# Performance work log

Measured on AMD Instinct MI355X. Metric: run time of the kernel, lower is better.

The kernel has to match this reference:

```python
import jax, jax.numpy as jnp
import numpy as np
from functools import partial

VOCAB, EMB, HID, B, T, K = 30000, 256, 512, 128, 256, 12
START, STOP = 10, 11


def lstm_scan(xs, mask, W_ih, W_hh, b_ih, b_hh, h0, c0):
    """xs: [T,B,E], mask: [T,B] bool. PyTorch gate order i,f,g,o. Masked steps carry state (packed-seq semantics)."""
    def step(carry, inp):
        h, c = carry
        x_t, m_t = inp
        gates = x_t @ W_ih.T + h @ W_hh.T + (b_ih + b_hh)  # [B,4H]
        i, f, g, o = jnp.split(gates, 4, axis=-1)
        c_new = jax.nn.sigmoid(f) * c + jax.nn.sigmoid(i) * jnp.tanh(g)
        h_new = jax.nn.sigmoid(o) * jnp.tanh(c_new)
        m = m_t[:, None]
        h = jnp.where(m, h_new, h)
        c = jnp.where(m, c_new, c)
        return (h, c), h
    _, hs = jax.lax.scan(step, (h0, c0), (xs, mask))
    return hs  # [T,B,H]


def crf_log_partition(emissions, mask, trans):
    """emissions: [T,B,K], mask: [T,B]. Vectorized log-sum-exp forward algorithm."""
    b, k = emissions.shape[1], emissions.shape[2]
    alpha0 = jnp.full((b, k), -10000.0, emissions.dtype).at[:, START].set(0.0)
    def step(alpha, inp):
        emit_t, m_t = inp
        # alpha_new[b,j] = logsumexp_i(alpha[b,i] + trans[j,i]) + emit[b,j]
        scores = alpha[:, None, :] + trans[None, :, :]  # [B,Knext,Kprev]
        alpha_new = jax.nn.logsumexp(scores, axis=-1) + emit_t
        return jnp.where(m_t[:, None], alpha_new, alpha), None
    alpha, _ = jax.lax.scan(step, alpha0, (emissions, mask))
    return jax.nn.logsumexp(alpha + trans[STOP][None, :], axis=-1)  # [B]


def crf_gold_score(emissions_bt, tags, lengths, trans):
    """emissions_bt: [B,T,K]. Gold path score with <start> prepended and <stop> transition."""
    b, t = tags.shape
    tags_ext = jnp.concatenate([jnp.full((b, 1), START, tags.dtype), tags], axis=1)  # [B,T+1]
    prev, nxt = tags_ext[:, :-1], tags_ext[:, 1:]  # [B,T]
    trans_s = trans[nxt, prev]  # [B,T]
    emit_s = jnp.take_along_axis(emissions_bt, nxt[:, :, None], axis=2)[:, :, 0]  # [B,T]
    valid = jnp.arange(t)[None, :] < lengths[:, None]  # [B,T]
    score = jnp.sum(jnp.where(valid, trans_s + emit_s, 0.0), axis=1)
    last_tag = jnp.take_along_axis(tags, (lengths - 1)[:, None], axis=1)[:, 0]
    return score + trans[STOP, last_tag]


def setup_inputs() -> dict:
    key = jax.random.key(0)
    ks = jax.random.split(key, 16)
    s = 0.1
    x = jax.random.randint(ks[0], (B, T), 0, VOCAB)
    lengths = jax.random.randint(ks[1], (B,), 1, T + 1)
    tags = jax.random.randint(ks[2], (B, T), 0, K - 2)  # real labels only
    embedding = jax.random.normal(ks[3], (VOCAB, EMB), jnp.float32) * s
    W_ih_f = jax.random.normal(ks[4], (4 * HID, EMB), jnp.float32) * s
    W_hh_f = jax.random.normal(ks[5], (4 * HID, HID), jnp.float32) * s
    b_ih_f = jax.random.normal(ks[6], (4 * HID,), jnp.float32) * s
    b_hh_f = jax.random.normal(ks[7], (4 * HID,), jnp.float32) * s
    W_ih_b = jax.random.normal(ks[8], (4 * HID, EMB), jnp.float32) * s
    W_hh_b = jax.random.normal(ks[9], (4 * HID, HID), jnp.float32) * s
    b_ih_b = jax.random.normal(ks[10], (4 * HID,), jnp.float32) * s
    b_hh_b = jax.random.normal(ks[11], (4 * HID,), jnp.float32) * s
    fc_W = jax.random.normal(ks[12], (K, 2 * HID), jnp.float32) * s
    fc_b = jnp.zeros((K,), jnp.float32)
    trans = jax.random.normal(ks[13], (K, K), jnp.float32) * s
    trans = trans.at[START, :].set(-10000.0).at[:, STOP].set(-10000.0)
    h0 = jax.random.normal(ks[14], (2, B, HID), jnp.float32) * s
    c0 = jax.random.normal(ks[15], (2, B, HID), jnp.float32) * s
    return dict(x=x, lengths=lengths, tags=tags, embedding=embedding,
                W_ih_f=W_ih_f, W_hh_f=W_hh_f, b_ih_f=b_ih_f, b_hh_f=b_hh_f,
                W_ih_b=W_ih_b, W_hh_b=W_hh_b, b_ih_b=b_ih_b, b_hh_b=b_hh_b,
                fc_W=fc_W, fc_b=fc_b, trans=trans, h0=h0, c0=c0)


def reference(x, lengths, tags, embedding, W_ih_f, W_hh_f, b_ih_f, b_hh_f,
              W_ih_b, W_hh_b, b_ih_b, b_hh_b, fc_W, fc_b, trans, h0, c0):
    # neg_log_likelihood: BiLSTM emission feats -> CRF logZ - gold score. Dropout = eval (identity).
    emb = embedding[x]                 # [B,T,E]
    xs = emb.transpose(1, 0, 2)        # [T,B,E] time-major
    t = xs.shape[0]
    mask = jnp.arange(t)[:, None] < lengths[None, :]  # [T,B]
    hs_f = lstm_scan(xs, mask, W_ih_f, W_hh_f, b_ih_f, b_hh_f, h0[0], c0[0])
    hs_b = lstm_scan(xs[::-1], mask[::-1], W_ih_b, W_hh_b, b_ih_b, b_hh_b, h0[1], c0[1])[::-1]
    out = jnp.concatenate([hs_f, hs_b], axis=-1)      # [T,B,2H]
    emissions = out @ fc_W.T + fc_b                    # [T,B,K]
    log_z = crf_log_partition(emissions, mask, trans)  # [B]
    gold = crf_gold_score(emissions.transpose(1, 0, 2), tags, lengths, trans)  # [B]
    return log_z - gold  # per-sentence NLL, [B]
```

## Files before the change

kernel.cpp:

```cpp
#include <hip/hip_runtime.h>
#include <hip/hip_bf16.h>

#define TT 256
#define BB 128
#define EMBD 256
#define HID 512
#define KTAG 12
#define START_TAG 10
#define STOP_TAG 11
#define SMEM_BYTES 148608

typedef __attribute__((ext_vector_type(8))) short short8;
typedef __attribute__((ext_vector_type(4))) float f32x4;

__device__ __forceinline__ unsigned short f2bf(float f) {
    union { float f; unsigned int u; } v; v.f = f;
    unsigned int r = v.u + 0x7fffu + ((v.u >> 16) & 1u);
    return (unsigned short)(r >> 16);
}
__device__ __forceinline__ float fsig(float x) {
    return __fdividef(1.0f, 1.0f + __expf(-x));
}
__device__ __forceinline__ float ftanh(float x) {
    return 2.0f * __fdividef(1.0f, 1.0f + __expf(-2.0f * x)) - 1.0f;
}
__device__ __forceinline__ void gll16(const void* g, void* l) {
    __builtin_amdgcn_global_load_lds((const __attribute__((address_space(1))) void*)g,
                                     (__attribute__((address_space(3))) void*)l, 16, 0, 0);
}
__device__ __forceinline__ void pack8(const float* src, unsigned short* dst) {
    float4 v0 = *(const float4*)src;
    float4 v1 = *(const float4*)(src + 4);
    unsigned short tmp[8];
    tmp[0] = f2bf(v0.x); tmp[1] = f2bf(v0.y); tmp[2] = f2bf(v0.z); tmp[3] = f2bf(v0.w);
    tmp[4] = f2bf(v1.x); tmp[5] = f2bf(v1.y); tmp[6] = f2bf(v1.z); tmp[7] = f2bf(v1.w);
    *(uint4*)dst = *(const uint4*)tmp;
}

#define SCHED_FENCE() __builtin_amdgcn_sched_barrier(0)
#define WAIT_VM4() do { asm volatile("s_waitcnt vmcnt(4)" ::: "memory"); SCHED_FENCE(); } while (0)
#define WAIT_VM0() do { asm volatile("s_waitcnt vmcnt(0)" ::: "memory"); SCHED_FENCE(); } while (0)
#define BARRIER_RAW() do { __builtin_amdgcn_s_barrier(); SCHED_FENCE(); } while (0)

__global__ void prologue(const int* __restrict__ x, const float* __restrict__ emb,
                         const float* __restrict__ Wihf, const float* __restrict__ Whhf,
                         const float* __restrict__ Wihb, const float* __restrict__ Whhb,
                         const float* __restrict__ h0,
                         const float* __restrict__ bihf, const float* __restrict__ bhhf,
                         const float* __restrict__ bihb, const float* __restrict__ bhhb,
                         const float* __restrict__ fcW,
                         unsigned short* __restrict__ xs, unsigned short* __restrict__ Wr,
                         unsigned short* __restrict__ h0buf, float* __restrict__ bias2,
                         unsigned short* __restrict__ fcWr, unsigned int* __restrict__ ctrl)
{
    int blk = blockIdx.x;
    int tid = threadIdx.x;
    if (blk < 4096) {
        int i = blk * 256 + tid;
        int chk = i & 31;
        int row = i >> 5;
        int b = row & (BB - 1);
        int t = row >> 7;
        pack8(emb + (size_t)x[b * TT + t] * EMBD + chk * 8, xs + (size_t)row * EMBD + chk * 8);
    } else if (blk < 5632) {
        int i = (blk - 4096) * 256 + tid;
        int c8 = i % 96;
        int r2 = i / 96;
        int nr = r2 & 2047;
        int dir = r2 >> 11;
        int utile = nr >> 6;
        int r6 = nr & 63;
        int wm = r6 >> 4;
        int rr = r6 & 15;
        int ul = rr >> 2, g = rr & 3;
        int orow = g * HID + utile * 16 + wm * 4 + ul;
        int k0 = c8 * 8;
        const float* Wih = dir ? Wihb : Wihf;
        const float* Whh = dir ? Whhb : Whhf;
        const float* src = (k0 < EMBD) ? (Wih + (size_t)orow * EMBD + k0)
                                       : (Whh + (size_t)orow * HID + (k0 - EMBD));
        pack8(src, Wr + ((size_t)dir * 2048 + nr) * 768 + k0);
    } else {
        int i = (blk - 5632) * 256 + tid;
        if (i < 2 * BB * HID) h0buf[i] = f2bf(h0[i]);
        if (i < 2 * 2048) {
            int dir = i >> 11, j = i & 2047;
            bias2[i] = dir ? (bihb[j] + bhhb[j]) : (bihf[j] + bhhf[j]);
        }
        if (i < 16 * 1024) {
            int tag = i >> 10, k = i & 1023;
            fcWr[i] = f2bf(tag < KTAG ? fcW[tag * 1024 + k] : 0.0f);
        }
        if (i < 2048) ctrl[i] = 0u;
    }
}

__launch_bounds__(256, 1)
__global__ void lstm_persistent(
    const unsigned short* __restrict__ xs, const unsigned short* __restrict__ Wr,
    const float* __restrict__ bias2, const int* __restrict__ lengths,
    const unsigned short* __restrict__ h0buf, const float* __restrict__ c0,
    unsigned short* __restrict__ hsf, unsigned short* __restrict__ hsb,
    unsigned int* __restrict__ ctrl)
{
    extern __shared__ char smem[];
    unsigned short* Wlds = (unsigned short*)smem;
    unsigned short* Abuf = (unsigned short*)(smem + 98304);
    unsigned short* hrep = (unsigned short*)(smem + 147456);

    const int blk = blockIdx.x;
    const int grp = blk & 7;
    const int dir = grp >> 2;
    const int btile = grp & 3;
    const int utile = blk >> 3;
    const int bg0 = btile * 32;

    const int tid = threadIdx.x;
    const int w = tid >> 6;
    const int l = tid & 63;
    const int l15 = l & 15, l16 = l >> 4;

    unsigned int* wflags = ctrl + 64 + grp * 128;
    unsigned int* myflag = wflags + utile * 4 + w;

    unsigned short* hs = dir ? hsb : hsf;
    unsigned int* hs_u32 = (unsigned int*)hs;

    {
        const unsigned short* src0 =
            Wr + ((size_t)(dir * 2048 + utile * 64) + (w * 16 + l15)) * 768 + l16 * 8;
        #pragma unroll
        for (int ks = 0; ks < 24; ks++)
            gll16(src0 + ks * 32, Wlds + (w * 24 + ks) * 512);
    }
    {
        int mm = w & 1, ksb = (w >> 1) * 4;
        const int t0 = dir ? (TT - 1) : 0;
        const unsigned short* asrc =
            xs + ((size_t)t0 * BB + (bg0 + mm * 16 + l15)) * EMBD + l16 * 8;
        #pragma unroll
        for (int q = 0; q < 4; q++)
            gll16(asrc + (ksb + q) * 32, Abuf + (mm * 24 + ksb + q) * 512);
    }

    const int u = utile * 16 + w * 4 + l16;
    const int bA = bg0 + l15, bB = bg0 + 16 + l15;
    const int lenA = lengths[bA], lenB = lengths[bB];
    float cA = c0[((size_t)dir * BB + bA) * HID + u];
    float cB = c0[((size_t)dir * BB + bB) * HID + u];
    float bias_r[4];
    #pragma unroll
    for (int g = 0; g < 4; g++) bias_r[g] = bias2[dir * 2048 + g * 512 + u];

    for (int s = 0; s < TT; s++) {
        const int t = dir ? (TT - 1 - s) : s;

        __syncthreads();

        f32x4 aA0 = {bias_r[0], bias_r[1], bias_r[2], bias_r[3]};
        f32x4 aB0 = {bias_r[0], bias_r[1], bias_r[2], bias_r[3]};
        f32x4 aA1 = {0.f,0.f,0.f,0.f}, aB1 = {0.f,0.f,0.f,0.f};
        auto mstep = [&](int ks, f32x4& xA, f32x4& xB) {
            short8 a  = *(const short8*)(Wlds + ((w * 24 + ks) << 9) + (l << 3));
            short8 b0 = *(const short8*)(Abuf + (ks << 9) + (l << 3));
            short8 b1 = *(const short8*)(Abuf + ((24 + ks) << 9) + (l << 3));
            xA = __builtin_amdgcn_mfma_f32_16x16x32_bf16(a, b0, xA, 0, 0, 0);
            xB = __builtin_amdgcn_mfma_f32_16x16x32_bf16(a, b1, xB, 0, 0, 0);
        };
        #pragma unroll
        for (int ks = 0; ks < 8; ks += 2) { mstep(ks, aA0, aB0); mstep(ks + 1, aA1, aB1); }

        if (s > 0) {
            if (tid < 64) {
                unsigned tgt = (unsigned)s;
                const unsigned long long* fp =
                    (const unsigned long long*)(wflags + 2 * (tid & 63));
                unsigned long long v0 = __hip_atomic_load(fp, __ATOMIC_RELAXED,
                                                          __HIP_MEMORY_SCOPE_AGENT);
                unsigned long long v1 = __hip_atomic_load(fp, __ATOMIC_RELAXED,
                                                          __HIP_MEMORY_SCOPE_AGENT);
                while (true) {
                    bool ok = ((unsigned)v0 >= tgt) && ((unsigned)(v0 >> 32) >= tgt);
                    if (__all(ok)) break;
                    v0 = v1;
                    v1 = __hip_atomic_load(fp, __ATOMIC_RELAXED, __HIP_MEMORY_SCOPE_AGENT);
                }
            }
            __syncthreads();
        }
        const unsigned short* hsrc = (s == 0)
            ? (h0buf + (size_t)dir * BB * HID)
            : (hs + (size_t)(dir ? (t + 1) : (t - 1)) * BB * HID);

        {
            int mm = w & 1, ksb = 8 + (w >> 1) * 8;
            const unsigned short* asrcH = hsrc + (size_t)(bg0 + mm * 16 + l15) * HID + l16 * 8;
            #pragma unroll
            for (int q = 0; q < 8; q++)
                gll16(asrcH + ((ksb + q) * 32 - 256), Abuf + (mm * 24 + ksb + q) * 512);
        }
        SCHED_FENCE();
        WAIT_VM4();
        BARRIER_RAW();
        #pragma unroll
        for (int q = 0; q < 4; q++) { mstep(8 + q, aA0, aB0); mstep(16 + q, aA1, aB1); }
        WAIT_VM0();
        BARRIER_RAW();
        #pragma unroll
        for (int q = 0; q < 4; q++) { mstep(12 + q, aA0, aB0); mstep(20 + q, aA1, aB1); }
        f32x4 accA = aA0 + aA1;
        f32x4 accB = aB0 + aB1;

        {
            const int ksn = 8 + (u >> 5), kin = u & 31;
            const int baseA = ksn * 512 + ((kin >> 3) * 16 + l15) * 8 + (kin & 7);
            const int baseB = (24 + ksn) * 512 + ((kin >> 3) * 16 + l15) * 8 + (kin & 7);
            float cnA = fsig(accA[1]) * cA + fsig(accA[0]) * ftanh(accA[2]);
            float hnA = fsig(accA[3]) * ftanh(cnA);
            float cnB = fsig(accB[1]) * cB + fsig(accB[0]) * ftanh(accB[2]);
            float hnB = fsig(accB[3]) * ftanh(cnB);
            bool mA = t < lenA, mB = t < lenB;
            unsigned short hvA = mA ? f2bf(hnA) : Abuf[baseA];
            unsigned short hvB = mB ? f2bf(hnB) : Abuf[baseB];
            cA = mA ? cnA : cA;
            cB = mB ? cnB : cB;
            hrep[l15 * 18 + w * 4 + l16]        = hvA;
            hrep[(16 + l15) * 18 + w * 4 + l16] = hvB;
        }
        __syncthreads();

        {
            int bl = tid >> 3, up = tid & 7;
            unsigned v0 = hrep[bl * 18 + up * 2];
            unsigned v1 = hrep[bl * 18 + up * 2 + 1];
            unsigned pk = v0 | (v1 << 16);
            size_t widx = (((size_t)t * BB + (bg0 + bl)) * HID + utile * 16 + up * 2) >> 1;
            __hip_atomic_store(hs_u32 + widx, pk, __ATOMIC_RELAXED, __HIP_MEMORY_SCOPE_AGENT);
        }
        SCHED_FENCE();
        if (s < TT - 1) {
            const int tn = dir ? (TT - 2 - s) : (s + 1);
            int mm = w & 1, ksb = (w >> 1) * 4;
            const unsigned short* asrc =
                xs + ((size_t)tn * BB + (bg0 + mm * 16 + l15)) * EMBD + l16 * 8;
            #pragma unroll
            for (int q = 0; q < 4; q++)
                gll16(asrc + (ksb + q) * 32, Abuf + (mm * 24 + ksb + q) * 512);
            SCHED_FENCE();
            WAIT_VM4();
            if (l == 0)
                __hip_atomic_store(myflag, (unsigned)(s + 1), __ATOMIC_RELAXED,
                                   __HIP_MEMORY_SCOPE_AGENT);
        }
    }
}

__global__ void emissions_mfma(const unsigned short* __restrict__ hsf,
                               const unsigned short* __restrict__ hsb,
                               const unsigned short* __restrict__ fcWr,
                               const float* __restrict__ fcb, float* __restrict__ emis)
{
    __shared__ unsigned short Wl[16 * 1024];
    int tid = threadIdx.x;
    #pragma unroll
    for (int p = 0; p < 8; p++) {
        int i = (p * 256 + tid) * 8;
        *(uint4*)(Wl + i) = *(const uint4*)(fcWr + i);
    }
    __syncthreads();
    int w = tid >> 6, l = tid & 63;
    int l15 = l & 15, l16 = l >> 4;
    float bval = fcb[l15 < KTAG ? l15 : 0];
    #pragma unroll
    for (int tile = 0; tile < 2; tile++) {
        int rowbase = ((blockIdx.x * 4 + w) * 2 + tile) * 16;
        f32x4 acc0 = {0.f,0.f,0.f,0.f}, acc1 = {0.f,0.f,0.f,0.f};
        auto estep = [&](const unsigned short* hsp, int ks, f32x4& acc) {
            short8 av = *(const short8*)(hsp + (size_t)(rowbase + l15) * HID + (ks & 15) * 32 + l16 * 8);
            short8 bv = *(const short8*)(Wl + l15 * 1024 + ks * 32 + l16 * 8);
            acc = __builtin_amdgcn_mfma_f32_16x16x32_bf16(av, bv, acc, 0, 0, 0);
        };
        #pragma unroll
        for (int ks = 0; ks < 16; ks += 2) { estep(hsf, ks, acc0); estep(hsf, ks + 1, acc1); }
        #pragma unroll
        for (int ks = 16; ks < 32; ks += 2) { estep(hsb, ks, acc0); estep(hsb, ks + 1, acc1); }
        f32x4 acc = acc0 + acc1;
        if (l15 < KTAG) {
            #pragma unroll
            for (int r = 0; r < 4; r++)
                emis[(size_t)(rowbase + 4 * l16 + r) * KTAG + l15] = acc[r] + bval;
        }
    }
}

__global__ void crf_gold(const float* __restrict__ emis, const int* __restrict__ lengths,
                         const int* __restrict__ tags, const float* __restrict__ trans,
                         float* __restrict__ out)
{
    __shared__ float s_logz, s_gold;
    int b = blockIdx.x;
    int tid = threadIdx.x;
    int len = lengths[b];
    if (tid < 64) {
        int lane = tid;
        float trow[KTAG];
        #pragma unroll
        for (int j = 0; j < KTAG; j++)
            trow[j] = (lane < KTAG) ? trans[lane * KTAG + j] : -1e30f;
        float alpha = (lane == START_TAG) ? 0.0f : -10000.0f;
        float e_cur = (lane < KTAG) ? emis[(size_t)b * KTAG + lane] : 0.0f;
        for (int t = 0; t < len; t++) {
            int tn = (t + 1 < TT) ? t + 1 : t;
            float e_next = (lane < KTAG) ? emis[(size_t)(tn * BB + b) * KTAG + lane] : 0.0f;
            float sc[KTAG];
            #pragma unroll
            for (int j = 0; j < KTAG; j++) sc[j] = __shfl(alpha, j, 64) + trow[j];
            float m = sc[0];
            #pragma unroll
            for (int j = 1; j < KTAG; j++) m = fmaxf(m, sc[j]);
            float ssum = 0.0f;
            #pragma unroll
            for (int j = 0; j < KTAG; j++) ssum += __expf(sc[j] - m);
            float anew = m + __logf(ssum) + e_cur;
            alpha = (lane < KTAG) ? anew : alpha;
            e_cur = e_next;
        }
        float v = (lane < KTAG) ? (alpha + trans[STOP_TAG * KTAG + lane]) : -1e30f;
        float m = v;
        #pragma unroll
        for (int off = 1; off < 16; off <<= 1) m = fmaxf(m, __shfl_xor(m, off, 64));
        float e = __expf(v - m);
        #pragma unroll
        for (int off = 1; off < 16; off <<= 1) e += __shfl_xor(e, off, 64);
        if (lane == 0) s_logz = m + __logf(e);
    } else {
        int l2 = tid - 64;
        float part = 0.0f;
        #pragma unroll
        for (int q = 0; q < 4; q++) {
            int t = l2 + q * 64;
            if (t < len) {
                int nxt = tags[b * TT + t];
                int prev = t ? tags[b * TT + t - 1] : START_TAG;
                part += trans[nxt * KTAG + prev] + emis[(size_t)(t * BB + b) * KTAG + nxt];
            }
        }
        #pragma unroll
        for (int off = 1; off < 64; off <<= 1) part += __shfl_xor(part, off, 64);
        if (l2 == 0) s_gold = part + trans[STOP_TAG * KTAG + tags[b * TT + len - 1]];
    }
    __syncthreads();
    if (tid == 0) out[b] = s_logz - s_gold;
}

extern "C" void kernel_launch(void* const* d_in, const int* in_sizes, int n_in,
                              void* d_out, int out_size, void* d_ws, size_t ws_size,
                              hipStream_t stream)
{
    (void)in_sizes; (void)n_in; (void)out_size; (void)ws_size;
    const int*   x     = (const int*)d_in[0];
    const int*   lens  = (const int*)d_in[1];
    const int*   tags  = (const int*)d_in[2];
    const float* emb   = (const float*)d_in[3];
    const float* Wihf  = (const float*)d_in[4];
    const float* Whhf  = (const float*)d_in[5];
    const float* bihf  = (const float*)d_in[6];
    const float* bhhf  = (const float*)d_in[7];
    const float* Wihb  = (const float*)d_in[8];
    const float* Whhb  = (const float*)d_in[9];
    const float* bihb  = (const float*)d_in[10];
    const float* bhhb  = (const float*)d_in[11];
    const float* fcW   = (const float*)d_in[12];
    const float* fcb   = (const float*)d_in[13];
    const float* trans = (const float*)d_in[14];
    const float* h0    = (const float*)d_in[15];
    const float* c0    = (const float*)d_in[16];
    float* out = (float*)d_out;

    char* ws = (char*)d_ws;
    size_t off = 0;
    auto alloc = [&](size_t bytes) {
        void* p = ws + off;
        off += (bytes + 255) & ~(size_t)255;
        return p;
    };
    unsigned short* xs    = (unsigned short*)alloc((size_t)TT * BB * EMBD * 2);
    unsigned short* Wr    = (unsigned short*)alloc((size_t)2 * 2048 * 768 * 2);
    float*          bias2 = (float*)alloc((size_t)2 * 2048 * 4);
    unsigned short* h0buf = (unsigned short*)alloc((size_t)2 * BB * HID * 2);
    unsigned short* hsf   = (unsigned short*)alloc((size_t)TT * BB * HID * 2);
    unsigned short* hsb   = (unsigned short*)alloc((size_t)TT * BB * HID * 2);
    float*          emis  = (float*)alloc((size_t)TT * BB * KTAG * 4);
    unsigned short* fcWr  = (unsigned short*)alloc((size_t)16 * 1024 * 2);
    unsigned int*   ctrl  = (unsigned int*)alloc((size_t)2048 * 4);

    prologue<<<6144, 256, 0, stream>>>(x, emb, Wihf, Whhf, Wihb, Whhb, h0,
                                       bihf, bhhf, bihb, bhhb, fcW,
                                       xs, Wr, h0buf, bias2, fcWr, ctrl);

    hipFuncSetAttribute(reinterpret_cast<const void*>(lstm_persistent),
                        hipFuncAttributeMaxDynamicSharedMemorySize, SMEM_BYTES);
    {
        const unsigned short* p_xs = xs; const unsigned short* p_Wr = Wr;
        const float* p_bias2 = bias2; const int* p_lens = lens;
        const unsigned short* p_h0 = h0buf; const float* p_c0 = c0;
        unsigned short* p_hsf = hsf; unsigned short* p_hsb = hsb;
        unsigned int* p_ctrl = ctrl;
        void* args[9] = { &p_xs, &p_Wr, &p_bias2, &p_lens, &p_h0, &p_c0,
                          &p_hsf, &p_hsb, &p_ctrl };
        hipError_t e = hipLaunchCooperativeKernel(
            reinterpret_cast<const void*>(lstm_persistent),
            dim3(256), dim3(256), args, (unsigned)SMEM_BYTES, stream);
        if (e != hipSuccess) {
            lstm_persistent<<<256, 256, SMEM_BYTES, stream>>>(
                xs, Wr, bias2, lens, h0buf, c0, hsf, hsb, ctrl);
        }
    }

    emissions_mfma<<<256, 256, 0, stream>>>(hsf, hsb, fcWr, fcb, emis);
    crf_gold<<<BB, 128, 0, stream>>>(emis, lens, tags, trans, out);
}
```

Baseline: 1.068 ms.

## Repartition persistent LSTM blocks to 8 hidden units over two interleaved batch tiles

Each persistent block now owns 8 hidden units (32 gate rows) for two 32-row batch tiles of one direction, instead of 16 units for a single batch tile. The block alternates between the two tiles inside each timestep, so waiting on cross-block flags for one tile can overlap with compute on the other. The weight tile in LDS halves, the x and h staging buffers are split and double-buffered per tile, and the weight prepack layout changes to match. The cost is twice as many flag waits and barriers per step, and each wave does half the MFMA work per phase, which may expose more latency.

```diff
diff --git a/kernel.cpp b/kernel.cpp
--- a/kernel.cpp
+++ b/kernel.cpp
@@ -8,10 +8,11 @@
 #define KTAG 12
 #define START_TAG 10
 #define STOP_TAG 11
-#define SMEM_BYTES 148608
+#define SMEM_BYTES 117248
 
 typedef __attribute__((ext_vector_type(8))) short short8;
 typedef __attribute__((ext_vector_type(4))) float f32x4;
+typedef unsigned long long ull;
 
 __device__ __forceinline__ unsigned short f2bf(float f) {
     union { float f; unsigned int u; } v; v.f = f;
@@ -68,12 +69,12 @@
         int r2 = i / 96;
         int nr = r2 & 2047;
         int dir = r2 >> 11;
-        int utile = nr >> 6;
-        int r6 = nr & 63;
-        int wm = r6 >> 4;
-        int rr = r6 & 15;
+        int U = nr >> 5;
+        int r5 = nr & 31;
+        int nsub = r5 >> 4;
+        int rr = r5 & 15;
         int ul = rr >> 2, g = rr & 3;
-        int orow = g * HID + utile * 16 + wm * 4 + ul;
+        int orow = g * HID + U * 8 + nsub * 4 + ul;
         int k0 = c8 * 8;
         const float* Wih = dir ? Wihb : Wihf;
         const float* Whh = dir ? Whhb : Whhf;
@@ -105,152 +106,160 @@
 {
     extern __shared__ char smem[];
     unsigned short* Wlds = (unsigned short*)smem;
-    unsigned short* Abuf = (unsigned short*)(smem + 98304);
-    unsigned short* hrep = (unsigned short*)(smem + 147456);
+    unsigned short* Ah   = (unsigned short*)(smem + 49152);
+    unsigned short* Axs[2] = { (unsigned short*)(smem + 81920),
+                               (unsigned short*)(smem + 98304) };
+    unsigned short* hrp[2] = { (unsigned short*)(smem + 114688),
+                               (unsigned short*)(smem + 115968) };
 
     const int blk = blockIdx.x;
-    const int grp = blk & 7;
-    const int dir = grp >> 2;
-    const int btile = grp & 3;
-    const int utile = blk >> 3;
-    const int bg0 = btile * 32;
+    const int dir = blk & 1;
+    const int p   = (blk >> 1) & 1;
+    const int U   = blk >> 2;
 
     const int tid = threadIdx.x;
     const int w = tid >> 6;
     const int l = tid & 63;
     const int l15 = l & 15, l16 = l >> 4;
-
-    unsigned int* wflags = ctrl + 64 + grp * 128;
-    unsigned int* myflag = wflags + utile * 4 + w;
+    const int m = w & 1, n = w >> 1;
+
+    const int bg0[2] = { (p * 2) * 32, (p * 2 + 1) * 32 };
+    unsigned int* flbase[2] = { ctrl + 64 + (dir * 4 + p * 2) * 128,
+                                ctrl + 64 + (dir * 4 + p * 2 + 1) * 128 };
 
     unsigned short* hs = dir ? hsb : hsf;
     unsigned int* hs_u32 = (unsigned int*)hs;
 
     {
-        const unsigned short* src0 =
-            Wr + ((size_t)(dir * 2048 + utile * 64) + (w * 16 + l15)) * 768 + l16 * 8;
-        #pragma unroll
-        for (int ks = 0; ks < 24; ks++)
-            gll16(src0 + ks * 32, Wlds + (w * 24 + ks) * 512);
+        #pragma unroll
+        for (int cc = 0; cc < 12; cc++) {
+            int c = w * 12 + cc;
+            int nsub = c / 24, ks = c % 24;
+            const unsigned short* src =
+                Wr + ((size_t)(dir * 2048 + U * 32 + nsub * 16) + l15) * 768 + ks * 32 + l16 * 8;
+            gll16(src, Wlds + c * 512);
+        }
     }
     {
-        int mm = w & 1, ksb = (w >> 1) * 4;
         const int t0 = dir ? (TT - 1) : 0;
-        const unsigned short* asrc =
-            xs + ((size_t)t0 * BB + (bg0 + mm * 16 + l15)) * EMBD + l16 * 8;
-        #pragma unroll
-        for (int q = 0; q < 4; q++)
-            gll16(asrc + (ksb + q) * 32, Abuf + (mm * 24 + ksb + q) * 512);
-    }
-
-    const int u = utile * 16 + w * 4 + l16;
-    const int bA = bg0 + l15, bB = bg0 + 16 + l15;
-    const int lenA = lengths[bA], lenB = lengths[bB];
-    float cA = c0[((size_t)dir * BB + bA) * HID + u];
-    float cB = c0[((size_t)dir * BB + bB) * HID + u];
+        #pragma unroll
+        for (int ch = 0; ch < 2; ch++) {
+            int mm = w & 1, ksb = (w >> 1) * 4;
+            const unsigned short* asrc =
+                xs + ((size_t)t0 * BB + (bg0[ch] + mm * 16 + l15)) * EMBD + l16 * 8;
+            #pragma unroll
+            for (int q = 0; q < 4; q++)
+                gll16(asrc + (ksb + q) * 32, Axs[ch] + (mm * 8 + ksb + q) * 512);
+        }
+    }
+
+    const int u = U * 8 + n * 4 + l16;
+    const int b_local = m * 16 + l15;
+    int len_r[2]; float c_reg[2];
+    #pragma unroll
+    for (int ch = 0; ch < 2; ch++) {
+        len_r[ch] = lengths[bg0[ch] + b_local];
+        c_reg[ch] = c0[((size_t)dir * BB + bg0[ch] + b_local) * HID + u];
+    }
     float bias_r[4];
     #pragma unroll
     for (int g = 0; g < 4; g++) bias_r[g] = bias2[dir * 2048 + g * 512 + u];
 
     for (int s = 0; s < TT; s++) {
         const int t = dir ? (TT - 1 - s) : s;
-
-        __syncthreads();
-
-        f32x4 aA0 = {bias_r[0], bias_r[1], bias_r[2], bias_r[3]};
-        f32x4 aB0 = {bias_r[0], bias_r[1], bias_r[2], bias_r[3]};
-        f32x4 aA1 = {0.f,0.f,0.f,0.f}, aB1 = {0.f,0.f,0.f,0.f};
-        auto mstep = [&](int ks, f32x4& xA, f32x4& xB) {
-            short8 a  = *(const short8*)(Wlds + ((w * 24 + ks) << 9) + (l << 3));
-            short8 b0 = *(const short8*)(Abuf + (ks << 9) + (l << 3));
-            short8 b1 = *(const short8*)(Abuf + ((24 + ks) << 9) + (l << 3));
-            xA = __builtin_amdgcn_mfma_f32_16x16x32_bf16(a, b0, xA, 0, 0, 0);
-            xB = __builtin_amdgcn_mfma_f32_16x16x32_bf16(a, b1, xB, 0, 0, 0);
-        };
-        #pragma unroll
-        for (int ks = 0; ks < 8; ks += 2) { mstep(ks, aA0, aB0); mstep(ks + 1, aA1, aB1); }
-
-        if (s > 0) {
-            if (tid < 64) {
-                unsigned tgt = (unsigned)s;
-                const unsigned long long* fp =
-                    (const unsigned long long*)(wflags + 2 * (tid & 63));
-                unsigned long long v0 = __hip_atomic_load(fp, __ATOMIC_RELAXED,
-                                                          __HIP_MEMORY_SCOPE_AGENT);
-                unsigned long long v1 = __hip_atomic_load(fp, __ATOMIC_RELAXED,
-                                                          __HIP_MEMORY_SCOPE_AGENT);
-                while (true) {
-                    bool ok = ((unsigned)v0 >= tgt) && ((unsigned)(v0 >> 32) >= tgt);
-                    if (__all(ok)) break;
-                    v0 = v1;
-                    v1 = __hip_atomic_load(fp, __ATOMIC_RELAXED, __HIP_MEMORY_SCOPE_AGENT);
+        #pragma unroll
+        for (int ch = 0; ch < 2; ch++) {
+            __syncthreads();
+
+            f32x4 a0 = { bias_r[0], bias_r[1], bias_r[2], bias_r[3] };
+            f32x4 a1 = { 0.f, 0.f, 0.f, 0.f };
+            auto mstep = [&](int ks, f32x4& acc) {
+                short8 av = *(const short8*)(Wlds + ((n * 24 + ks) << 9) + (l << 3));
+                const unsigned short* bp = (ks < 8)
+                    ? (Axs[ch] + ((m * 8 + ks) << 9))
+                    : (Ah + ((m * 16 + (ks - 8)) << 9));
+                short8 bv = *(const short8*)(bp + (l << 3));
+                acc = __builtin_amdgcn_mfma_f32_16x16x32_bf16(av, bv, acc, 0, 0, 0);
+            };
+            #pragma unroll
+            for (int ks = 0; ks < 8; ks += 2) { mstep(ks, a0); mstep(ks + 1, a1); }
+
+            if (s > 0) {
+                if (tid < 64) {
+                    unsigned tgt = (unsigned)s;
+                    const ull* fp = (const ull*)(flbase[ch] + 2 * (tid & 63));
+                    ull v0 = __hip_atomic_load(fp, __ATOMIC_RELAXED, __HIP_MEMORY_SCOPE_AGENT);
+                    ull v1 = __hip_atomic_load(fp, __ATOMIC_RELAXED, __HIP_MEMORY_SCOPE_AGENT);
+                    while (true) {
+                        bool ok = ((unsigned)v0 >= tgt) && ((unsigned)(v0 >> 32) >= tgt);
+                        if (__all(ok)) break;
+                        v0 = v1;
+                        v1 = __hip_atomic_load(fp, __ATOMIC_RELAXED, __HIP_MEMORY_SCOPE_AGENT);
+                    }
                 }
-            }
-            __syncthreads();
-        }
-        const unsigned short* hsrc = (s == 0)
-            ? (h0buf + (size_t)dir * BB * HID)
-            : (hs + (size_t)(dir ? (t + 1) : (t - 1)) * BB * HID);
-
-        {
-            int mm = w & 1, ksb = 8 + (w >> 1) * 8;
-            const unsigned short* asrcH = hsrc + (size_t)(bg0 + mm * 16 + l15) * HID + l16 * 8;
-            #pragma unroll
-            for (int q = 0; q < 8; q++)
-                gll16(asrcH + ((ksb + q) * 32 - 256), Abuf + (mm * 24 + ksb + q) * 512);
-        }
-        SCHED_FENCE();
-        WAIT_VM4();
-        BARRIER_RAW();
-        #pragma unroll
-        for (int q = 0; q < 4; q++) { mstep(8 + q, aA0, aB0); mstep(16 + q, aA1, aB1); }
-        WAIT_VM0();
-        BARRIER_RAW();
-        #pragma unroll
-        for (int q = 0; q < 4; q++) { mstep(12 + q, aA0, aB0); mstep(20 + q, aA1, aB1); }
-        f32x4 accA = aA0 + aA1;
-        f32x4 accB = aB0 + aB1;
-
-        {
-            const int ksn = 8 + (u >> 5), kin = u & 31;
-            const int baseA = ksn * 512 + ((kin >> 3) * 16 + l15) * 8 + (kin & 7);
-            const int baseB = (24 + ksn) * 512 + ((kin >> 3) * 16 + l15) * 8 + (kin & 7);
-            float cnA = fsig(accA[1]) * cA + fsig(accA[0]) * ftanh(accA[2]);
-            float hnA = fsig(accA[3]) * ftanh(cnA);
-            float cnB = fsig(accB[1]) * cB + fsig(accB[0]) * ftanh(accB[2]);
-            float hnB = fsig(accB[3]) * ftanh(cnB);
-            bool mA = t < lenA, mB = t < lenB;
-            unsigned short hvA = mA ? f2bf(hnA) : Abuf[baseA];
-            unsigned short hvB = mB ? f2bf(hnB) : Abuf[baseB];
-            cA = mA ? cnA : cA;
-            cB = mB ? cnB : cB;
-            hrep[l15 * 18 + w * 4 + l16]        = hvA;
-            hrep[(16 + l15) * 18 + w * 4 + l16] = hvB;
-        }
-        __syncthreads();
-
-        {
-            int bl = tid >> 3, up = tid & 7;
-            unsigned v0 = hrep[bl * 18 + up * 2];
-            unsigned v1 = hrep[bl * 18 + up * 2 + 1];
-            unsigned pk = v0 | (v1 << 16);
-            size_t widx = (((size_t)t * BB + (bg0 + bl)) * HID + utile * 16 + up * 2) >> 1;
-            __hip_atomic_store(hs_u32 + widx, pk, __ATOMIC_RELAXED, __HIP_MEMORY_SCOPE_AGENT);
-        }
-        SCHED_FENCE();
-        if (s < TT - 1) {
-            const int tn = dir ? (TT - 2 - s) : (s + 1);
-            int mm = w & 1, ksb = (w >> 1) * 4;
-            const unsigned short* asrc =
-                xs + ((size_t)tn * BB + (bg0 + mm * 16 + l15)) * EMBD + l16 * 8;
-            #pragma unroll
-            for (int q = 0; q < 4; q++)
-                gll16(asrc + (ksb + q) * 32, Abuf + (mm * 24 + ksb + q) * 512);
+                __syncthreads();
+            }
+            const unsigned short* hsrc = (s == 0)
+                ? (h0buf + (size_t)dir * BB * HID)
+                : (hs + (size_t)(dir ? (t + 1) : (t - 1)) * BB * HID);
+
+            {
+                int mm = w & 1, ksb = (w >> 1) * 8;
+                const unsigned short* aH =
+                    hsrc + (size_t)(bg0[ch] + mm * 16 + l15) * HID + l16 * 8;
+                #pragma unroll
+                for (int q = 0; q < 8; q++)
+                    gll16(aH + (ksb + q) * 32, Ah + (mm * 16 + ksb + q) * 512);
+            }
             SCHED_FENCE();
             WAIT_VM4();
-            if (l == 0)
-                __hip_atomic_store(myflag, (unsigned)(s + 1), __ATOMIC_RELAXED,
+            BARRIER_RAW();
+            #pragma unroll
+            for (int q = 0; q < 4; q++) { mstep(8 + q, a0); mstep(16 + q, a1); }
+            WAIT_VM0();
+            BARRIER_RAW();
+            #pragma unroll
+            for (int q = 0; q < 4; q++) { mstep(12 + q, a0); mstep(20 + q, a1); }
+            f32x4 acc = a0 + a1;
+
+            {
+                const int kk = 256 + u;
+                const int ksn = (kk >> 5) - 8, kin = kk & 31;
+                unsigned short carried =
+                    Ah[(m * 16 + ksn) * 512 + ((kin >> 3) * 16 + l15) * 8 + (kin & 7)];
+                bool msk = t < len_r[ch];
+                float cn = fsig(acc[1]) * c_reg[ch] + fsig(acc[0]) * ftanh(acc[2]);
+                float hn = fsig(acc[3]) * ftanh(cn);
+                unsigned short hv = msk ? f2bf(hn) : carried;
+                c_reg[ch] = msk ? cn : c_reg[ch];
+                hrp[ch][b_local * 18 + n * 4 + l16] = hv;
+            }
+            __syncthreads();
+
+            if (tid < 128) {
+                int row = tid >> 2, up = tid & 3;
+                unsigned v0 = hrp[ch][row * 18 + up * 2];
+                unsigned v1 = hrp[ch][row * 18 + up * 2 + 1];
+                unsigned pk = v0 | (v1 << 16);
+                size_t widx = (((size_t)t * BB + bg0[ch] + row) * HID + U * 8 + up * 2) >> 1;
+                __hip_atomic_store(hs_u32 + widx, pk, __ATOMIC_RELAXED,
                                    __HIP_MEMORY_SCOPE_AGENT);
+            }
+            SCHED_FENCE();
+            if (s < TT - 1) {
+                const int tn = dir ? (t - 1) : (t + 1);
+                int mm = w & 1, ksb = (w >> 1) * 4;
+                const unsigned short* asrc =
+                    xs + ((size_t)tn * BB + (bg0[ch] + mm * 16 + l15)) * EMBD + l16 * 8;
+                #pragma unroll
+                for (int q = 0; q < 4; q++)
+                    gll16(asrc + (ksb + q) * 32, Axs[ch] + (mm * 8 + ksb + q) * 512);
+                SCHED_FENCE();
+                WAIT_VM4();
+                if (w < 2 && l == 0)
+                    __hip_atomic_store(flbase[ch] + U * 2 + w, (unsigned)(s + 1),
+                                       __ATOMIC_RELAXED, __HIP_MEMORY_SCOPE_AGENT);
+            }
         }
     }
 }
```

Measured after the change: 1.737 ms. 62.6% more time.
